# Optimization experiments

Hardware: AMD Instinct MI355X
Metric: run time of the kernel (lower is better)

The kernel has to match this reference:

```python
import jax, jax.numpy as jnp
import numpy as np

D = 1024      # d_model
ED = 2048     # d_inner
K = 4         # d_conv
N = 16        # d_state
R = 64        # dt_rank
E = 8         # num_experts
TOPK = 2      # num_experts_per_tok
FF = 2048     # mlp_size
EPS = 1e-6
B, L = 1, 2048


def setup_inputs() -> dict:
    key = jax.random.key(0)
    ks = jax.random.split(key, 12)
    def nrm(k, shape, scale=0.02):
        return jax.random.normal(k, shape, jnp.float32) * scale
    return {
        "x": jax.random.normal(ks[0], (B, L, D), jnp.float32),
        "rms1_w": jnp.ones((D,), jnp.float32),
        "rms2_w": jnp.ones((D,), jnp.float32),
        "W_in": nrm(ks[1], (2 * ED, D)),
        "conv_w": nrm(ks[2], (ED, 1, K), 0.1),
        "conv_b": jnp.zeros((ED,), jnp.float32),
        "W_xproj": nrm(ks[3], (R + 2 * N, ED)),
        "W_dt": nrm(ks[4], (ED, R), 0.1),
        "b_dt": jnp.full((ED,), -4.6, jnp.float32),  # softplus(-4.6) ~ 0.01 init dt
        "A_log": jnp.log(jnp.tile(jnp.arange(1, N + 1, dtype=jnp.float32), (ED, 1))),  # S4D-real init
        "D_skip": jnp.ones((ED,), jnp.float32),
        "W_out": nrm(ks[5], (D, ED)),
        "W_router": nrm(ks[6], (E, D)),
        "gate_w": nrm(ks[7], (E, FF, D)),
        "up_w": nrm(ks[8], (E, FF, D)),
        "down_w": nrm(ks[9], (E, D, FF)),
    }


def rmsnorm(x, w):
    return x * jax.lax.rsqrt(jnp.mean(x * x, -1, keepdims=True) + EPS) * w


def mamba(x, W_in, conv_w, conv_b, W_xproj, W_dt, b_dt, A_log, D_skip, W_out):
    Bb, Ll, _ = x.shape
    xm, z = jnp.split(x @ W_in.T, 2, axis=-1)                 # [B,L,ED] each
    # depthwise causal conv over time
    xc = jax.lax.conv_general_dilated(xm.transpose(0, 2, 1), conv_w, (1,), [(K - 1, 0)],
                                      feature_group_count=ED)  # [B,ED,L]
    xc = jax.nn.silu((xc + conv_b[None, :, None]).transpose(0, 2, 1))  # [B,L,ED]
    dt, Bm, Cm = jnp.split(xc @ W_xproj.T, [R, R + N], axis=-1)        # [B,L,R],[B,L,N],[B,L,N]
    delta = jax.nn.softplus(dt @ W_dt.T + b_dt)                        # [B,L,ED]
    A = -jnp.exp(A_log)                                                # [ED,N]
    dA = jnp.exp(delta[..., None] * A)                                 # [B,L,ED,N]
    dBx = delta[..., None] * Bm[:, :, None, :] * xc[..., None]         # [B,L,ED,N]

    def step(h, t):
        dA_t, dBx_t, C_t = t
        h = dA_t * h + dBx_t
        return h, jnp.einsum("ben,bn->be", h, C_t)

    h0 = jnp.zeros((Bb, ED, N), x.dtype)
    _, ys = jax.lax.scan(step, h0, (dA.transpose(1, 0, 2, 3), dBx.transpose(1, 0, 2, 3), Cm.transpose(1, 0, 2)))
    y = ys.transpose(1, 0, 2) + D_skip * xc
    y = y * jax.nn.silu(z)
    return y @ W_out.T


def moe(x2d, W_router, gate_w, up_w, down_w):
    logits = x2d @ W_router.T                                  # [T,E]
    probs = jax.nn.softmax(logits.astype(jnp.float32), -1)
    topw, sel = jax.lax.top_k(probs, TOPK)                     # NOTE: no renormalization (faithful)
    topw = topw.astype(x2d.dtype)
    wmat = jnp.sum(jax.nn.one_hot(sel, E, dtype=x2d.dtype) * topw[..., None], axis=1)  # [T,E]
    g = jnp.einsum("td,efd->tef", x2d, gate_w)
    u = jnp.einsum("td,efd->tef", x2d, up_w)
    h = jax.nn.silu(g) * u
    ye = jnp.einsum("tef,edf->ted", h, down_w)
    out = jnp.einsum("ted,te->td", ye, wmat)
    return out, logits


def reference(x, rms1_w, rms2_w, W_in, conv_w, conv_b, W_xproj, W_dt, b_dt, A_log,
              D_skip, W_out, W_router, gate_w, up_w, down_w):
    Bb, Ll, Dd = x.shape
    res = x
    h = rmsnorm(x, rms1_w)
    h = mamba(h, W_in, conv_w, conv_b, W_xproj, W_dt, b_dt, A_log, D_skip, W_out)
    x = res + h
    res = x
    h = rmsnorm(x, rms2_w)
    mo, logits = moe(h.reshape(-1, Dd), W_router, gate_w, up_w, down_w)
    x = res + mo.reshape(Bb, Ll, Dd)
    return (x, logits)
```

## Files before the change

kernel.cpp:

```cpp
#include <hip/hip_runtime.h>
#include <math.h>

typedef unsigned short u16;
typedef unsigned int   u32;
typedef __attribute__((ext_vector_type(8))) short bf16x8;
typedef __attribute__((ext_vector_type(4))) float f32x4;

constexpr int Tn=2048, Dm=1024, EDc=2048, Ns=16, Rr=64, NEx=8, FFc=2048;
constexpr int SCH=32, SNCH=Tn/SCH;
constexpr int MAXTM=40;
constexpr int MAXTM2=24;
constexpr float LOG2E = 1.44269504f;

__device__ __forceinline__ float siluf(float x){ return __fdividef(x, 1.f + __expf(-x)); }
__device__ __forceinline__ u16 bfr(float f){
  u32 u = __float_as_uint(f);
  return (u16)((u + 0x7fffu + ((u>>16)&1u)) >> 16);
}
__device__ __forceinline__ float b2f(u16 h){ return __uint_as_float(((u32)h)<<16); }

__device__ __forceinline__ void gload16(const void* g, void* l){
  __builtin_amdgcn_global_load_lds((const __attribute__((address_space(1))) void*)g,
                                   (__attribute__((address_space(3))) void*)l, 16, 0, 0);
}

__global__ __launch_bounds__(256) void f2b_k(const float* __restrict__ in,
                                             u16* __restrict__ out, int n4){
  int i = blockIdx.x*256 + threadIdx.x;
  if (i >= n4) return;
  float4 v = ((const float4*)in)[i];
  u32 lo = (u32)bfr(v.x) | ((u32)bfr(v.y)<<16);
  u32 hi = (u32)bfr(v.z) | ((u32)bfr(v.w)<<16);
  ((uint2*)out)[i] = make_uint2(lo, hi);
}

__global__ __launch_bounds__(256) void f2b3_k(
    const float* __restrict__ g, const float* __restrict__ u,
    const float* __restrict__ d,
    u16* __restrict__ og, u16* __restrict__ ou, u16* __restrict__ od){
  const int BPW = (NEx*FFc*Dm/4)/256;
  int b = blockIdx.x;
  int which = b / BPW;
  int i = (b - which*BPW)*256 + threadIdx.x;
  const float* in = (which==0) ? g : (which==1) ? u : d;
  u16* out        = (which==0) ? og : (which==1) ? ou : od;
  float4 v = ((const float4*)in)[i];
  u32 lo = (u32)bfr(v.x) | ((u32)bfr(v.y)<<16);
  u32 hi = (u32)bfr(v.z) | ((u32)bfr(v.w)<<16);
  ((uint2*)out)[i] = make_uint2(lo, hi);
}

__global__ __launch_bounds__(256) void rmsnorm_k(const float* __restrict__ x,
                                                 const float* __restrict__ w,
                                                 u16* __restrict__ ob){
  int t = blockIdx.x;
  const float* xr = x + (size_t)t * Dm;
  float v[4]; float s = 0.f;
#pragma unroll
  for (int j = 0; j < 4; j++){ int d = threadIdx.x + j*256; v[j] = xr[d]; s += v[j]*v[j]; }
#pragma unroll
  for (int m = 1; m < 64; m <<= 1) s += __shfl_xor(s, m);
  __shared__ float red[4]; __shared__ float sb;
  int lane = threadIdx.x & 63, wv = threadIdx.x >> 6;
  if (lane == 0) red[wv] = s;
  __syncthreads();
  if (threadIdx.x == 0) sb = rsqrtf((red[0]+red[1]+red[2]+red[3]) * (1.f/Dm) + 1e-6f);
  __syncthreads();
  float sc = sb;
#pragma unroll
  for (int j = 0; j < 4; j++){
    int d = threadIdx.x + j*256;
    ob[(size_t)t*Dm + d] = bfr(v[j]*sc*w[d]);
  }
}

__global__ __launch_bounds__(256) void rms2red_k(
  const float* __restrict__ x, const float* __restrict__ P,
  const float* __restrict__ w,
  float* __restrict__ out, float* __restrict__ h2f, u16* __restrict__ h2b)
{
  int t = blockIdx.x, tid = threadIdx.x;
  const size_t S = (size_t)Tn*Dm;
  float v[4]; float s = 0.f;
#pragma unroll
  for (int j = 0; j < 4; j++){
    int d = tid + j*256;
    size_t idx = (size_t)t*Dm + d;
    float a = x[idx] + ((P[idx] + P[S+idx]) + (P[2*S+idx] + P[3*S+idx]));
    out[idx] = a; v[j] = a; s += a*a;
  }
#pragma unroll
  for (int m = 1; m < 64; m <<= 1) s += __shfl_xor(s, m);
  __shared__ float red[4]; __shared__ float sb;
  int lane = tid & 63, wv = tid >> 6;
  if (lane == 0) red[wv] = s;
  __syncthreads();
  if (tid == 0) sb = rsqrtf((red[0]+red[1]+red[2]+red[3]) * (1.f/Dm) + 1e-6f);
  __syncthreads();
  float sc = sb;
#pragma unroll
  for (int j = 0; j < 4; j++){
    int d = tid + j*256;
    float o = v[j]*sc*w[d];
    h2b[(size_t)t*Dm + d] = bfr(o);
    h2f[(size_t)t*Dm + d] = o;
  }
}

template<int EPI, int OB>
__global__ __launch_bounds__(512) void gemm_bb(
    const u16* __restrict__ A, int lda,
    const u16* __restrict__ B, int ldb,
    void* __restrict__ Cv, int ldc,
    int M, int N, int Ksl, const float* __restrict__ aux)
{
  __shared__ u16 As[2*4096], Bs[2*4096];
  int tid = threadIdx.x, lane = tid & 63, wid = tid >> 6;
  int wr = wid >> 2, wc = wid & 3;
  int n0 = blockIdx.x * 128, m0 = blockIdx.y * 128;
  int r = tid >> 2;
  int kk = ((tid & 3) ^ (r & 3)) * 8;
  size_t kbeg = (size_t)blockIdx.z * Ksl;
  const u16* Ag = A + (size_t)min(m0 + r, M-1)*lda + kbeg + kk;
  const u16* Bg = B + (size_t)min(n0 + r, N-1)*ldb + kbeg + kk;
  f32x4 acc[4][2] = {};
  int sw = ((lane>>4) ^ (lane&3)) * 8;
  int aoff[4], boff[2];
#pragma unroll
  for (int i = 0; i < 4; i++) aoff[i] = (wr*64 + i*16 + (lane&15))*32 + sw;
#pragma unroll
  for (int j = 0; j < 2; j++) boff[j] = (wc*32 + j*16 + (lane&15))*32 + sw;
  gload16(Ag, As + tid*8);
  gload16(Bg, Bs + tid*8);
  int NT = Ksl >> 5;
  for (int kt = 0; kt < NT; kt++){
    int cur = (kt & 1) * 4096;
    if (kt + 1 < NT){
      int nxt = 4096 - cur;
      gload16(Ag + (size_t)(kt+1)*32, As + nxt + tid*8);
      gload16(Bg + (size_t)(kt+1)*32, Bs + nxt + tid*8);
      asm volatile("s_waitcnt vmcnt(2)" ::: "memory");
    } else {
      asm volatile("s_waitcnt vmcnt(0)" ::: "memory");
    }
    __builtin_amdgcn_s_barrier();
    bf16x8 af[4], bv[2];
#pragma unroll
    for (int i = 0; i < 4; i++) af[i] = *(const bf16x8*)&As[cur + aoff[i]];
#pragma unroll
    for (int j = 0; j < 2; j++) bv[j] = *(const bf16x8*)&Bs[cur + boff[j]];
    asm volatile("s_waitcnt lgkmcnt(0)" ::: "memory");
    __builtin_amdgcn_sched_barrier(0);
    __builtin_amdgcn_s_barrier();
    __builtin_amdgcn_s_setprio(1);
#pragma unroll
    for (int i = 0; i < 4; i++)
#pragma unroll
      for (int j = 0; j < 2; j++)
        acc[i][j] = __builtin_amdgcn_mfma_f32_16x16x32_bf16(af[i], bv[j], acc[i][j], 0,0,0);
    __builtin_amdgcn_s_setprio(0);
  }
  float* Cf = (float*)Cv + (size_t)blockIdx.z * M * ldc;
  u16*   Cb = (u16*)Cv;
#pragma unroll
  for (int i = 0; i < 4; i++){
    int rbase = m0 + wr*64 + i*16 + ((lane>>4)<<2);
#pragma unroll
    for (int j = 0; j < 2; j++){
      int col = n0 + wc*32 + j*16 + (lane&15);
      if (col >= N) continue;
#pragma unroll
      for (int q = 0; q < 4; q++){
        int row = rbase + q;
        if (row >= M) continue;
        float v = acc[i][j][q];
        if (EPI == 1){ v += aux[col]; v = (v > 20.f) ? v : __logf(1.f + __expf(v)); }
        if (OB) Cb[(size_t)row*ldc + col] = bfr(v);
        else    Cf[(size_t)row*ldc + col] = v;
      }
    }
  }
}

__global__ __launch_bounds__(512) void gateup8(
    const u16* __restrict__ Aall,
    const u16* __restrict__ Wg, const u16* __restrict__ Wu,
    const int* __restrict__ cnt, const int* __restrict__ off,
    const int* __restrict__ bucket,
    const int* __restrict__ tmap, const int* __restrict__ ntot,
    u16* __restrict__ H)
{
  if ((int)blockIdx.y >= *ntot) return;
  int v = tmap[blockIdx.y];
  int e = v >> 16, m0 = (v & 0xFFFF) * 256;
  int Me = cnt[e];
  __shared__ u16 As[2*8192], Gs[2*2048], Us[2*2048];
  int tid = threadIdx.x, lane = tid & 63, wid = tid >> 6;
  int wr = wid >> 1, wc = wid & 1;
  int n0 = blockIdx.x * 64;
  int r = tid >> 2;
  int kk = ((tid & 3) ^ (r & 3)) * 8;
  int arow  = bucket[e*Tn + min(m0 + r,       Me-1)];
  int arow2 = bucket[e*Tn + min(m0 + 128 + r, Me-1)];
  const u16* Ag  = Aall + (size_t)arow *Dm + kk;
  const u16* Ag2 = Aall + (size_t)arow2*Dm + kk;
  int rg = r & 63;
  const u16* GUg = ((tid < 256) ? Wg : Wu) + ((size_t)e*FFc + n0 + rg)*Dm + kk;
  u16* GUsb = (tid < 256) ? (u16*)Gs : (u16*)Us;
  int g8 = (tid & 255) * 8;
  f32x4 ag[4][2] = {}, au[4][2] = {};
  int sw = ((lane>>4) ^ (lane&3)) * 8;
  int aoff[4], boff[2];
#pragma unroll
  for (int i = 0; i < 4; i++) aoff[i] = (wr*64 + i*16 + (lane&15))*32 + sw;
#pragma unroll
  for (int j = 0; j < 2; j++) boff[j] = (wc*32 + j*16 + (lane&15))*32 + sw;
  const int NT = Dm >> 5;
  gload16(Ag,  As + tid*8);
  gload16(Ag2, As + 4096 + tid*8);
  gload16(GUg, GUsb + g8);
  for (int kt = 0; kt < NT; kt++){
    int cab = (kt & 1) * 8192, cgu = (kt & 1) * 2048;
    if (kt + 1 < NT){
      int nab = 8192 - cab, ngu = 2048 - cgu;
      gload16(Ag  + (size_t)(kt+1)*32, As + nab + tid*8);
      gload16(Ag2 + (size_t)(kt+1)*32, As + nab + 4096 + tid*8);
      gload16(GUg + (size_t)(kt+1)*32, GUsb + ngu + g8);
      asm volatile("s_waitcnt vmcnt(3)" ::: "memory");
    } else {
      asm volatile("s_waitcnt vmcnt(0)" ::: "memory");
    }
    __builtin_amdgcn_s_barrier();
    bf16x8 af[4], gf[2], uf[2];
#pragma unroll
    for (int i = 0; i < 4; i++) af[i] = *(const bf16x8*)&As[cab + aoff[i]];
#pragma unroll
    for (int j = 0; j < 2; j++){ gf[j] = *(const bf16x8*)&Gs[cgu + boff[j]];
                                 uf[j] = *(const bf16x8*)&Us[cgu + boff[j]]; }
    asm volatile("s_waitcnt lgkmcnt(0)" ::: "memory");
    __builtin_amdgcn_sched_barrier(0);
    __builtin_amdgcn_s_barrier();
    __builtin_amdgcn_s_setprio(1);
#pragma unroll
    for (int i = 0; i < 4; i++)
#pragma unroll
      for (int j = 0; j < 2; j++){
        ag[i][j] = __builtin_amdgcn_mfma_f32_16x16x32_bf16(af[i], gf[j], ag[i][j], 0,0,0);
        au[i][j] = __builtin_amdgcn_mfma_f32_16x16x32_bf16(af[i], uf[j], au[i][j], 0,0,0);
      }
    __builtin_amdgcn_s_setprio(0);
  }
  int offe = off[e];
#pragma unroll
  for (int i = 0; i < 4; i++){
    int mb = m0 + wr*64 + i*16 + ((lane>>4)<<2);
#pragma unroll
    for (int j = 0; j < 2; j++){
      int col = n0 + wc*32 + j*16 + (lane&15);
#pragma unroll
      for (int q = 0; q < 4; q++){
        int m = mb + q;
        if (m >= Me) continue;
        float g = ag[i][j][q], u = au[i][j][q];
        H[(size_t)(offe + m)*FFc + col] = bfr(siluf(g)*u);
      }
    }
  }
}

__global__ __launch_bounds__(512) void down8(
    const u16* __restrict__ Hall, const u16* __restrict__ Wd,
    const int* __restrict__ cnt, const int* __restrict__ off,
    const int* __restrict__ tmap2, const int* __restrict__ ntot2,
    u16* __restrict__ Y)
{
  if ((int)blockIdx.y >= *ntot2) return;
  int v = tmap2[blockIdx.y];
  int e = v >> 16, m0 = (v & 0xFFFF) * 128;
  int Me = cnt[e];
  int offe = off[e];
  int kbeg = blockIdx.z * (FFc/2);
  const u16* A = Hall + (size_t)offe*FFc;
  const u16* B = Wd + (size_t)e*Dm*FFc;
  u16* C = Y + (size_t)blockIdx.z*(2*Tn)*Dm + (size_t)offe*Dm;
  __shared__ u16 As[2*4096], Bs[2*4096];
  int tid = threadIdx.x, lane = tid & 63, wid = tid >> 6;
  int wr = wid >> 2, wc = wid & 3;
  int n0 = blockIdx.x * 128;
  int r = tid >> 2;
  int kk = ((tid & 3) ^ (r & 3)) * 8;
  const u16* Ag = A + (size_t)min(m0 + r, Me-1)*FFc + kbeg + kk;
  const u16* Bg = B + (size_t)(n0 + r)*FFc + kbeg + kk;
  f32x4 acc[4][2] = {};
  int sw = ((lane>>4) ^ (lane&3)) * 8;
  int aoff[4], boff[2];
#pragma unroll
  for (int i = 0; i < 4; i++) aoff[i] = (wr*64 + i*16 + (lane&15))*32 + sw;
#pragma unroll
  for (int j = 0; j < 2; j++) boff[j] = (wc*32 + j*16 + (lane&15))*32 + sw;
  gload16(Ag, As + tid*8);
  gload16(Bg, Bs + tid*8);
  const int NT = (FFc/2) >> 5;
  for (int kt = 0; kt < NT; kt++){
    int cur = (kt & 1) * 4096;
    if (kt + 1 < NT){
      int nxt = 4096 - cur;
      gload16(Ag + (size_t)(kt+1)*32, As + nxt + tid*8);
      gload16(Bg + (size_t)(kt+1)*32, Bs + nxt + tid*8);
      asm volatile("s_waitcnt vmcnt(2)" ::: "memory");
    } else {
      asm volatile("s_waitcnt vmcnt(0)" ::: "memory");
    }
    __builtin_amdgcn_s_barrier();
    bf16x8 af[4], bv[2];
#pragma unroll
    for (int i = 0; i < 4; i++) af[i] = *(const bf16x8*)&As[cur + aoff[i]];
#pragma unroll
    for (int j = 0; j < 2; j++) bv[j] = *(const bf16x8*)&Bs[cur + boff[j]];
    asm volatile("s_waitcnt lgkmcnt(0)" ::: "memory");
    __builtin_amdgcn_sched_barrier(0);
    __builtin_amdgcn_s_barrier();
    __builtin_amdgcn_s_setprio(1);
#pragma unroll
    for (int i = 0; i < 4; i++)
#pragma unroll
      for (int j = 0; j < 2; j++)
        acc[i][j] = __builtin_amdgcn_mfma_f32_16x16x32_bf16(af[i], bv[j], acc[i][j], 0,0,0);
    __builtin_amdgcn_s_setprio(0);
  }
#pragma unroll
  for (int i = 0; i < 4; i++){
    int mb = m0 + wr*64 + i*16 + ((lane>>4)<<2);
#pragma unroll
    for (int j = 0; j < 2; j++){
      int col = n0 + wc*32 + j*16 + (lane&15);
#pragma unroll
      for (int q = 0; q < 4; q++){
        int m = mb + q;
        if (m >= Me) continue;
        C[(size_t)m*Dm + col] = bfr(acc[i][j][q]);
      }
    }
  }
}

__global__ __launch_bounds__(256) void conv_k(const u16* __restrict__ xzb,
    const float* __restrict__ cw, const float* __restrict__ cb,
    u16* __restrict__ xc)
{
  int idx = blockIdx.x*256 + threadIdx.x;
  int t = idx >> 11, e = idx & (EDc - 1);
  float v = cb[e];
#pragma unroll
  for (int k = 0; k < 4; k++){
    int tt = t - 3 + k;
    if (tt >= 0) v += b2f(xzb[(size_t)tt*(2*EDc) + e]) * cw[e*4 + k];
  }
  xc[(size_t)t*EDc + e] = bfr(siluf(v));
}

__global__ __launch_bounds__(256) void xp_red(const float* __restrict__ part,
                                              float* __restrict__ xp,
                                              u16* __restrict__ dtA){
  int i = blockIdx.x*256 + threadIdx.x;
  const int S = Tn*96;
  float v = part[i] + part[S + i] + part[2*S + i] + part[3*S + i];
  xp[i] = v;
  int t = i / 96, c = i - t*96;
  if (c < Rr) dtA[t*Rr + c] = bfr(v);
}

__global__ __launch_bounds__(256) void scan_p1(
  const u16* __restrict__ delta, const u16* __restrict__ xc,
  const float* __restrict__ xp,  const float* __restrict__ A_log,
  float* __restrict__ hend, float* __restrict__ dsum)
{
  __shared__ u16 sdel[SCH*256], sxc[SCH*256];
  __shared__ float sB[SCH*16];
  int tid = threadIdx.x;
  int e0 = blockIdx.x*256, c = blockIdx.y, t0 = c*SCH;
#pragma unroll
  for (int i = 0; i < 4; i++){
    int f = (i*256+tid)*8;
    int t = f >> 8, e = f & 255;
    gload16(&delta[(size_t)(t0+t)*EDc + e0 + e], sdel + f);
    gload16(&xc  [(size_t)(t0+t)*EDc + e0 + e], sxc + f);
  }
  sB[tid]       = xp[(size_t)(t0 + (tid>>4))*96 + Rr + (tid&15)];
  sB[tid+256]   = xp[(size_t)(t0 + ((tid+256)>>4))*96 + Rr + (tid&15)];
  float a2[16];
  {
    const float* ar = &A_log[(size_t)(e0+tid)*16];
#pragma unroll
    for (int n = 0; n < 16; n++) a2[n] = -__expf(ar[n]) * LOG2E;
  }
  __syncthreads();
  float h[16] = {};
  float ds = 0.f;
  for (int t = 0; t < SCH; t++){
    float del = b2f(sdel[t*256 + tid]);
    float xv  = b2f(sxc [t*256 + tid]);
    ds += del;
    float dbx = del * xv;
    float4 b0 = *(const float4*)&sB[t*16];
    float4 b1 = *(const float4*)&sB[t*16+4];
    float4 b2 = *(const float4*)&sB[t*16+8];
    float4 b3 = *(const float4*)&sB[t*16+12];
    float bb[16] = {b0.x,b0.y,b0.z,b0.w, b1.x,b1.y,b1.z,b1.w,
                    b2.x,b2.y,b2.z,b2.w, b3.x,b3.y,b3.z,b3.w};
#pragma unroll
    for (int n = 0; n < 16; n++){
      float dA = exp2f(del * a2[n]);
      h[n] = fmaf(dA, h[n], dbx * bb[n]);
    }
  }
  float* hp = &hend[((size_t)c*EDc + e0 + tid)*16];
#pragma unroll
  for (int n = 0; n < 16; n += 4)
    *(float4*)&hp[n] = make_float4(h[n], h[n+1], h[n+2], h[n+3]);
  dsum[c*EDc + e0 + tid] = ds;
}

__global__ __launch_bounds__(256) void scan_p2(
  const float* __restrict__ hend, const float* __restrict__ dsum,
  const float* __restrict__ A_log, float* __restrict__ hin)
{
  int g = blockIdx.x*256 + threadIdx.x;
  int e = g >> 4;
  float a2 = -__expf(A_log[g]) * LOG2E;
  float h = 0.f;
  for (int c = 0; c < SNCH; c++){
    hin[(size_t)c*EDc*Ns + g] = h;
    float P = exp2f(a2 * dsum[c*EDc + e]);
    h = fmaf(P, h, hend[(size_t)c*EDc*Ns + g]);
  }
}

__global__ __launch_bounds__(256) void scan_p3(
  const u16* __restrict__ delta, const u16* __restrict__ xc,
  const float* __restrict__ xp,  const u16* __restrict__ xzb,
  const float* __restrict__ A_log, const float* __restrict__ D_skip,
  const float* __restrict__ hin,   u16* __restrict__ y2)
{
  __shared__ u16 sdel[SCH*256], sxc[SCH*256], sz[SCH*256];
  __shared__ float sB[SCH*16], sC[SCH*16];
  int tid = threadIdx.x;
  int e0 = blockIdx.x*256, c = blockIdx.y, t0 = c*SCH;
#pragma unroll
  for (int i = 0; i < 4; i++){
    int f = (i*256+tid)*8;
    int t = f >> 8, e = f & 255;
    gload16(&delta[(size_t)(t0+t)*EDc + e0 + e], sdel + f);
    gload16(&xc  [(size_t)(t0+t)*EDc + e0 + e], sxc + f);
    gload16(&xzb [(size_t)(t0+t)*(2*EDc) + EDc + e0 + e], sz + f);
  }
  {
    int f0 = tid, f1 = tid + 256;
    sB[f0] = xp[(size_t)(t0 + (f0>>4))*96 + Rr + (f0&15)];
    sB[f1] = xp[(size_t)(t0 + (f1>>4))*96 + Rr + (f1&15)];
    sC[f0] = xp[(size_t)(t0 + (f0>>4))*96 + Rr + Ns + (f0&15)];
    sC[f1] = xp[(size_t)(t0 + (f1>>4))*96 + Rr + Ns + (f1&15)];
  }
  float a2[16];
  {
    const float* ar = &A_log[(size_t)(e0+tid)*16];
#pragma unroll
    for (int n = 0; n < 16; n++) a2[n] = -__expf(ar[n]) * LOG2E;
  }
  float dsk = D_skip[e0 + tid];
  float h[16];
  {
    const float* hp = &hin[((size_t)c*EDc + e0 + tid)*16];
#pragma unroll
    for (int n = 0; n < 16; n += 4){
      float4 hv = *(const float4*)&hp[n];
      h[n] = hv.x; h[n+1] = hv.y; h[n+2] = hv.z; h[n+3] = hv.w;
    }
  }
  __syncthreads();
  for (int t = 0; t < SCH; t++){
    float del = b2f(sdel[t*256 + tid]);
    float xv  = b2f(sxc [t*256 + tid]);
    float zv  = b2f(sz  [t*256 + tid]);
    float dbx = del * xv;
    float4 b0 = *(const float4*)&sB[t*16];
    float4 b1 = *(const float4*)&sB[t*16+4];
    float4 b2 = *(const float4*)&sB[t*16+8];
    float4 b3 = *(const float4*)&sB[t*16+12];
    float bb[16] = {b0.x,b0.y,b0.z,b0.w, b1.x,b1.y,b1.z,b1.w,
                    b2.x,b2.y,b2.z,b2.w, b3.x,b3.y,b3.z,b3.w};
    float4 c0 = *(const float4*)&sC[t*16];
    float4 c1 = *(const float4*)&sC[t*16+4];
    float4 c2 = *(const float4*)&sC[t*16+8];
    float4 c3 = *(const float4*)&sC[t*16+12];
    float cc[16] = {c0.x,c0.y,c0.z,c0.w, c1.x,c1.y,c1.z,c1.w,
                    c2.x,c2.y,c2.z,c2.w, c3.x,c3.y,c3.z,c3.w};
    float p0 = 0.f, p1 = 0.f, p2 = 0.f, p3 = 0.f;
#pragma unroll
    for (int n = 0; n < 16; n += 4){
      float dA0 = exp2f(del * a2[n]);
      float dA1 = exp2f(del * a2[n+1]);
      float dA2 = exp2f(del * a2[n+2]);
      float dA3 = exp2f(del * a2[n+3]);
      h[n]   = fmaf(dA0, h[n],   dbx * bb[n]);
      h[n+1] = fmaf(dA1, h[n+1], dbx * bb[n+1]);
      h[n+2] = fmaf(dA2, h[n+2], dbx * bb[n+2]);
      h[n+3] = fmaf(dA3, h[n+3], dbx * bb[n+3]);
      p0 = fmaf(h[n],   cc[n],   p0);
      p1 = fmaf(h[n+1], cc[n+1], p1);
      p2 = fmaf(h[n+2], cc[n+2], p2);
      p3 = fmaf(h[n+3], cc[n+3], p3);
    }
    float p = (p0 + p1) + (p2 + p3);
    y2[(size_t)(t0+t)*EDc + e0 + tid] = bfr((p + dsk*xv) * siluf(zv));
  }
}

__global__ __launch_bounds__(256) void route_k(
  const float* __restrict__ h2, const float* __restrict__ Wr,
  float* __restrict__ logits_out,
  int* __restrict__ cnt, int* __restrict__ bucket,
  int* __restrict__ tok_e, int* __restrict__ tok_idx, float* __restrict__ tok_w)
{
  int t = blockIdx.x, tid = threadIdx.x;
  float p[8] = {};
#pragma unroll
  for (int j = 0; j < 4; j++){
    int d = tid + j*256;
    float xv = h2[(size_t)t*Dm + d];
#pragma unroll
    for (int e = 0; e < 8; e++) p[e] += xv * Wr[e*Dm + d];
  }
#pragma unroll
  for (int e = 0; e < 8; e++)
#pragma unroll
    for (int m = 1; m < 64; m <<= 1) p[e] += __shfl_xor(p[e], m);
  __shared__ float part[4][8];
  __shared__ float lg[8];
  int lane = tid & 63, wv = tid >> 6;
  if (lane == 0)
#pragma unroll
    for (int e = 0; e < 8; e++) part[wv][e] = p[e];
  __syncthreads();
  if (tid < 8){
    float v = part[0][tid]+part[1][tid]+part[2][tid]+part[3][tid];
    lg[tid] = v;
    logits_out[(size_t)t*8 + tid] = v;
  }
  __syncthreads();
  if (tid == 0){
    float mx = lg[0];
#pragma unroll
    for (int e = 1; e < 8; e++) mx = fmaxf(mx, lg[e]);
    float ex[8], s = 0.f;
#pragma unroll
    for (int e = 0; e < 8; e++){ ex[e] = expf(lg[e] - mx); s += ex[e]; }
    float inv = 1.f / s;
    int i0 = 0; float b0 = ex[0]*inv;
#pragma unroll
    for (int e = 1; e < 8; e++){ float pe = ex[e]*inv; if (pe > b0){ b0 = pe; i0 = e; } }
    int i1 = -1; float b1 = -1e30f;
#pragma unroll
    for (int e = 0; e < 8; e++){ if (e == i0) continue; float pe = ex[e]*inv; if (pe > b1){ b1 = pe; i1 = e; } }
    int k0 = atomicAdd(&cnt[i0], 1); bucket[i0*Tn + k0] = t;
    int k1 = atomicAdd(&cnt[i1], 1); bucket[i1*Tn + k1] = t;
    tok_e[2*t] = i0;   tok_idx[2*t] = k0;   tok_w[2*t] = b0;
    tok_e[2*t+1] = i1; tok_idx[2*t+1] = k1; tok_w[2*t+1] = b1;
  }
}

__global__ void prefix_k(const int* __restrict__ cnt, int* __restrict__ off,
                         int* __restrict__ tmap, int* __restrict__ ntot,
                         int* __restrict__ tmap2, int* __restrict__ ntot2){
  if (threadIdx.x == 0 && blockIdx.x == 0){
    int s = 0;
    for (int e = 0; e < NEx; e++){ off[e] = s; s += cnt[e]; }
    int nt = 0;
    for (int e = 0; e < NEx; e++){
      int tiles = (cnt[e] + 255) >> 8;
      for (int tm = 0; tm < tiles; tm++) tmap[nt++] = (e << 16) | tm;
    }
    *ntot = nt;
    int n2 = 0;
    for (int e = 0; e < NEx; e++){
      int tiles = (cnt[e] + 127) >> 7;
      for (int tm = 0; tm < tiles; tm++) tmap2[n2++] = (e << 16) | tm;
    }
    *ntot2 = n2;
  }
}

__global__ __launch_bounds__(256) void combine_k(float* __restrict__ out,
    const u16* __restrict__ Y, const int* __restrict__ off,
    const int* __restrict__ tok_e, const int* __restrict__ tok_idx,
    const float* __restrict__ tok_w)
{
  int t = blockIdx.x, tid = threadIdx.x;
  const size_t S2 = (size_t)(2*Tn)*Dm;
  int e0 = tok_e[2*t],   e1 = tok_e[2*t+1];
  size_t r0 = (size_t)(off[e0] + tok_idx[2*t])*Dm;
  size_t r1 = (size_t)(off[e1] + tok_idx[2*t+1])*Dm;
  float w0 = tok_w[2*t], w1 = tok_w[2*t+1];
#pragma unroll
  for (int j = 0; j < 4; j++){
    int d = tid + j*256;
    float y0 = b2f(Y[r0 + d]) + b2f(Y[S2 + r0 + d]);
    float y1 = b2f(Y[r1 + d]) + b2f(Y[S2 + r1 + d]);
    out[(size_t)t*Dm + d] += w0*y0 + w1*y1;
  }
}

extern "C" void kernel_launch(void* const* d_in, const int* in_sizes, int n_in,
                              void* d_out, int out_size, void* d_ws, size_t ws_size,
                              hipStream_t stream) {
  const float* x      = (const float*)d_in[0];
  const float* rms1_w = (const float*)d_in[1];
  const float* rms2_w = (const float*)d_in[2];
  const float* W_in   = (const float*)d_in[3];
  const float* conv_w = (const float*)d_in[4];
  const float* conv_b = (const float*)d_in[5];
  const float* W_xprj = (const float*)d_in[6];
  const float* W_dt   = (const float*)d_in[7];
  const float* b_dt   = (const float*)d_in[8];
  const float* A_log  = (const float*)d_in[9];
  const float* D_skip = (const float*)d_in[10];
  const float* W_out  = (const float*)d_in[11];
  const float* W_rt   = (const float*)d_in[12];
  const float* gate_w = (const float*)d_in[13];
  const float* up_w   = (const float*)d_in[14];
  const float* down_w = (const float*)d_in[15];

  float* out        = (float*)d_out;
  float* logits_out = out + (size_t)Tn*Dm;

  uint8_t* base = (uint8_t*)d_ws;
  size_t o = 0;
  auto alloc = [&](size_t bytes) -> void* {
    void* p = base + o;
    o = (o + bytes + 255) & ~(size_t)255;
    return p;
  };
  float* h2f   = (float*)alloc((size_t)Tn*Dm*4);
  u16*   h2b   = (u16*)  alloc((size_t)Tn*Dm*2);
  u16*   hmoe  = (u16*)  alloc((size_t)2*Tn*FFc*2);
  u16*   yslot = (u16*)  alloc((size_t)2*(2*Tn)*Dm*2);
  int*   cnt     = (int*)alloc(64);
  int*   off     = (int*)alloc(64);
  int*   ntot    = (int*)alloc(64);
  int*   ntot2   = (int*)alloc(64);
  int*   tmap    = (int*)alloc(MAXTM2*4 + 192);
  int*   tmap2   = (int*)alloc(MAXTM*4 + 192);
  int*   bucket  = (int*)alloc((size_t)NEx*Tn*4);
  int*   tok_e   = (int*)alloc((size_t)2*Tn*4);
  int*   tok_idx = (int*)alloc((size_t)2*Tn*4);
  float* tok_w   = (float*)alloc((size_t)2*Tn*4);
  size_t oz = o;
  u16*   xzb   = (u16*)  alloc((size_t)Tn*2*EDc*2);
  u16*   delta = (u16*)  alloc((size_t)Tn*EDc*2);
  u16*   xc    = (u16*)  alloc((size_t)Tn*EDc*2);
  u16*   y2    = (u16*)  alloc((size_t)Tn*EDc*2);
  u16*   h1b   = (u16*)  alloc((size_t)Tn*Dm*2);
  u16*   dtA   = (u16*)  alloc((size_t)Tn*Rr*2);
  float* xp    = (float*)alloc((size_t)Tn*96*4);
  float* xp_part=(float*)alloc((size_t)4*Tn*96*4);
  float* hend  = (float*)alloc((size_t)SNCH*EDc*Ns*4);
  float* hin   = (float*)alloc((size_t)SNCH*EDc*Ns*4);
  float* dsum  = (float*)alloc((size_t)SNCH*EDc*4);
  float* wpart = (float*)xzb;
  u16* wgate = (u16*)(base + oz);
  u16* wup   = wgate + (size_t)NEx*FFc*Dm;
  u16* wdown = wup   + (size_t)NEx*FFc*Dm;
  u16* wbin  = (u16*)yslot;
  u16* wbout = wbin + (size_t)2*EDc*Dm;
  u16* wxp   = (u16*)hmoe;
  u16* wdt   = wxp + (size_t)96*EDc;

  f2b_k<<<(2*EDc*Dm/4)/256, 256, 0, stream>>>(W_in,   wbin,  2*EDc*Dm/4);
  f2b_k<<<(Dm*EDc/4)/256,   256, 0, stream>>>(W_out,  wbout, Dm*EDc/4);
  f2b_k<<<(96*EDc/4)/256,   256, 0, stream>>>(W_xprj, wxp,   96*EDc/4);
  f2b_k<<<(EDc*Rr/4)/256,   256, 0, stream>>>(W_dt,   wdt,   EDc*Rr/4);
  rmsnorm_k<<<Tn, 256, 0, stream>>>(x, rms1_w, h1b);
  gemm_bb<0,1><<<dim3(32,16,1), 512, 0, stream>>>(h1b, Dm, wbin, Dm, xzb, 2*EDc, Tn, 2*EDc, Dm, nullptr);
  conv_k<<<(Tn*EDc)/256, 256, 0, stream>>>(xzb, conv_w, conv_b, xc);
  gemm_bb<0,0><<<dim3(1,16,4), 512, 0, stream>>>(xc, EDc, wxp, EDc, xp_part, 96, Tn, 96, EDc/4, nullptr);
  xp_red<<<(Tn*96)/256, 256, 0, stream>>>(xp_part, xp, dtA);
  gemm_bb<1,1><<<dim3(16,16,1), 512, 0, stream>>>(dtA, Rr, wdt, Rr, delta, EDc, Tn, EDc, Rr, b_dt);
  scan_p1<<<dim3(EDc/256, SNCH), 256, 0, stream>>>(delta, xc, xp, A_log, hend, dsum);
  scan_p2<<<EDc*Ns/256, 256, 0, stream>>>(hend, dsum, A_log, hin);
  scan_p3<<<dim3(EDc/256, SNCH), 256, 0, stream>>>(delta, xc, xp, xzb, A_log, D_skip, hin, y2);
  gemm_bb<0,0><<<dim3(8,16,4), 512, 0, stream>>>(y2, EDc, wbout, EDc, wpart, Dm, Tn, Dm, EDc/4, nullptr);
  rms2red_k<<<Tn, 256, 0, stream>>>(x, wpart, rms2_w, out, h2f, h2b);
  f2b3_k<<<3*((NEx*FFc*Dm/4)/256), 256, 0, stream>>>(gate_w, up_w, down_w, wgate, wup, wdown);
  hipMemsetAsync(cnt, 0, 32, stream);
  route_k<<<Tn, 256, 0, stream>>>(h2f, W_rt, logits_out, cnt, bucket, tok_e, tok_idx, tok_w);
  prefix_k<<<1, 64, 0, stream>>>(cnt, off, tmap, ntot, tmap2, ntot2);
  gateup8<<<dim3(32, MAXTM2), 512, 0, stream>>>(h2b, wgate, wup, cnt, off, bucket, tmap, ntot, hmoe);
  down8<<<dim3(8, MAXTM, 2), 512, 0, stream>>>(hmoe, wdown, cnt, off, tmap2, ntot2, yslot);
  combine_k<<<Tn, 256, 0, stream>>>(out, yslot, off, tok_e, tok_idx, tok_w);
}
```

Measured before the change: 397.2 us.

## Load MoE A-operand fragments directly from global into registers, bypassing LDS

```diff
diff --git a/kernel.cpp b/kernel.cpp
--- a/kernel.cpp
+++ b/kernel.cpp
@@ -194,46 +194,51 @@
   int v = tmap[blockIdx.y];
   int e = v >> 16, m0 = (v & 0xFFFF) * 256;
   int Me = cnt[e];
-  __shared__ u16 As[2*8192], Gs[2*2048], Us[2*2048];
+  __shared__ u16 Gs[2*2048], Us[2*2048];
   int tid = threadIdx.x, lane = tid & 63, wid = tid >> 6;
   int wr = wid >> 1, wc = wid & 1;
   int n0 = blockIdx.x * 64;
   int r = tid >> 2;
   int kk = ((tid & 3) ^ (r & 3)) * 8;
-  int arow  = bucket[e*Tn + min(m0 + r,       Me-1)];
-  int arow2 = bucket[e*Tn + min(m0 + 128 + r, Me-1)];
-  const u16* Ag  = Aall + (size_t)arow *Dm + kk;
-  const u16* Ag2 = Aall + (size_t)arow2*Dm + kk;
   int rg = r & 63;
   const u16* GUg = ((tid < 256) ? Wg : Wu) + ((size_t)e*FFc + n0 + rg)*Dm + kk;
   u16* GUsb = (tid < 256) ? (u16*)Gs : (u16*)Us;
   int g8 = (tid & 255) * 8;
+  const u16 *Af0, *Af1, *Af2, *Af3;
+  {
+    int kf = (lane >> 4) * 8;
+    int c  = lane & 15;
+    int r0 = bucket[e*Tn + min(m0 + wr*64 +  0 + c, Me-1)];
+    int r1 = bucket[e*Tn + min(m0 + wr*64 + 16 + c, Me-1)];
+    int r2 = bucket[e*Tn + min(m0 + wr*64 + 32 + c, Me-1)];
+    int r3 = bucket[e*Tn + min(m0 + wr*64 + 48 + c, Me-1)];
+    Af0 = Aall + (size_t)r0*Dm + kf;
+    Af1 = Aall + (size_t)r1*Dm + kf;
+    Af2 = Aall + (size_t)r2*Dm + kf;
+    Af3 = Aall + (size_t)r3*Dm + kf;
+  }
   f32x4 ag[4][2] = {}, au[4][2] = {};
   int sw = ((lane>>4) ^ (lane&3)) * 8;
-  int aoff[4], boff[2];
-#pragma unroll
-  for (int i = 0; i < 4; i++) aoff[i] = (wr*64 + i*16 + (lane&15))*32 + sw;
+  int boff[2];
 #pragma unroll
   for (int j = 0; j < 2; j++) boff[j] = (wc*32 + j*16 + (lane&15))*32 + sw;
   const int NT = Dm >> 5;
-  gload16(Ag,  As + tid*8);
-  gload16(Ag2, As + 4096 + tid*8);
   gload16(GUg, GUsb + g8);
   for (int kt = 0; kt < NT; kt++){
-    int cab = (kt & 1) * 8192, cgu = (kt & 1) * 2048;
+    int cgu = (kt & 1) * 2048;
+    bf16x8 af0 = *(const bf16x8*)(Af0 + (size_t)kt*32);
+    bf16x8 af1 = *(const bf16x8*)(Af1 + (size_t)kt*32);
+    bf16x8 af2 = *(const bf16x8*)(Af2 + (size_t)kt*32);
+    bf16x8 af3 = *(const bf16x8*)(Af3 + (size_t)kt*32);
+    __builtin_amdgcn_sched_barrier(0);
     if (kt + 1 < NT){
-      int nab = 8192 - cab, ngu = 2048 - cgu;
-      gload16(Ag  + (size_t)(kt+1)*32, As + nab + tid*8);
-      gload16(Ag2 + (size_t)(kt+1)*32, As + nab + 4096 + tid*8);
-      gload16(GUg + (size_t)(kt+1)*32, GUsb + ngu + g8);
-      asm volatile("s_waitcnt vmcnt(3)" ::: "memory");
+      gload16(GUg + (size_t)(kt+1)*32, GUsb + (2048 - cgu) + g8);
+      asm volatile("s_waitcnt vmcnt(5)" ::: "memory");
     } else {
-      asm volatile("s_waitcnt vmcnt(0)" ::: "memory");
+      asm volatile("s_waitcnt vmcnt(4)" ::: "memory");
     }
     __builtin_amdgcn_s_barrier();
-    bf16x8 af[4], gf[2], uf[2];
-#pragma unroll
-    for (int i = 0; i < 4; i++) af[i] = *(const bf16x8*)&As[cab + aoff[i]];
+    bf16x8 gf[2], uf[2];
 #pragma unroll
     for (int j = 0; j < 2; j++){ gf[j] = *(const bf16x8*)&Gs[cgu + boff[j]];
                                  uf[j] = *(const bf16x8*)&Us[cgu + boff[j]]; }
@@ -242,12 +247,16 @@
     __builtin_amdgcn_s_barrier();
     __builtin_amdgcn_s_setprio(1);
 #pragma unroll
-    for (int i = 0; i < 4; i++)
-#pragma unroll
-      for (int j = 0; j < 2; j++){
-        ag[i][j] = __builtin_amdgcn_mfma_f32_16x16x32_bf16(af[i], gf[j], ag[i][j], 0,0,0);
-        au[i][j] = __builtin_amdgcn_mfma_f32_16x16x32_bf16(af[i], uf[j], au[i][j], 0,0,0);
-      }
+    for (int j = 0; j < 2; j++){
+      ag[0][j] = __builtin_amdgcn_mfma_f32_16x16x32_bf16(af0, gf[j], ag[0][j], 0,0,0);
+      au[0][j] = __builtin_amdgcn_mfma_f32_16x16x32_bf16(af0, uf[j], au[0][j], 0,0,0);
+      ag[1][j] = __builtin_amdgcn_mfma_f32_16x16x32_bf16(af1, gf[j], ag[1][j], 0,0,0);
+      au[1][j] = __builtin_amdgcn_mfma_f32_16x16x32_bf16(af1, uf[j], au[1][j], 0,0,0);
+      ag[2][j] = __builtin_amdgcn_mfma_f32_16x16x32_bf16(af2, gf[j], ag[2][j], 0,0,0);
+      au[2][j] = __builtin_amdgcn_mfma_f32_16x16x32_bf16(af2, uf[j], au[2][j], 0,0,0);
+      ag[3][j] = __builtin_amdgcn_mfma_f32_16x16x32_bf16(af3, gf[j], ag[3][j], 0,0,0);
+      au[3][j] = __builtin_amdgcn_mfma_f32_16x16x32_bf16(af3, uf[j], au[3][j], 0,0,0);
+    }
     __builtin_amdgcn_s_setprio(0);
   }
   int offe = off[e];
@@ -283,38 +292,44 @@
   const u16* A = Hall + (size_t)offe*FFc;
   const u16* B = Wd + (size_t)e*Dm*FFc;
   u16* C = Y + (size_t)blockIdx.z*(2*Tn)*Dm + (size_t)offe*Dm;
-  __shared__ u16 As[2*4096], Bs[2*4096];
+  __shared__ u16 Bs[2*4096];
   int tid = threadIdx.x, lane = tid & 63, wid = tid >> 6;
   int wr = wid >> 2, wc = wid & 3;
   int n0 = blockIdx.x * 128;
   int r = tid >> 2;
   int kk = ((tid & 3) ^ (r & 3)) * 8;
-  const u16* Ag = A + (size_t)min(m0 + r, Me-1)*FFc + kbeg + kk;
   const u16* Bg = B + (size_t)(n0 + r)*FFc + kbeg + kk;
+  const u16 *Af0, *Af1, *Af2, *Af3;
+  {
+    int kf = (lane >> 4) * 8;
+    int c  = lane & 15;
+    Af0 = A + (size_t)min(m0 + wr*64 +  0 + c, Me-1)*FFc + kbeg + kf;
+    Af1 = A + (size_t)min(m0 + wr*64 + 16 + c, Me-1)*FFc + kbeg + kf;
+    Af2 = A + (size_t)min(m0 + wr*64 + 32 + c, Me-1)*FFc + kbeg + kf;
+    Af3 = A + (size_t)min(m0 + wr*64 + 48 + c, Me-1)*FFc + kbeg + kf;
+  }
   f32x4 acc[4][2] = {};
   int sw = ((lane>>4) ^ (lane&3)) * 8;
-  int aoff[4], boff[2];
-#pragma unroll
-  for (int i = 0; i < 4; i++) aoff[i] = (wr*64 + i*16 + (lane&15))*32 + sw;
+  int boff[2];
 #pragma unroll
   for (int j = 0; j < 2; j++) boff[j] = (wc*32 + j*16 + (lane&15))*32 + sw;
-  gload16(Ag, As + tid*8);
+  const int NT = (FFc/2) >> 5;
   gload16(Bg, Bs + tid*8);
-  const int NT = (FFc/2) >> 5;
   for (int kt = 0; kt < NT; kt++){
     int cur = (kt & 1) * 4096;
+    bf16x8 af0 = *(const bf16x8*)(Af0 + (size_t)kt*32);
+    bf16x8 af1 = *(const bf16x8*)(Af1 + (size_t)kt*32);
+    bf16x8 af2 = *(const bf16x8*)(Af2 + (size_t)kt*32);
+    bf16x8 af3 = *(const bf16x8*)(Af3 + (size_t)kt*32);
+    __builtin_amdgcn_sched_barrier(0);
     if (kt + 1 < NT){
-      int nxt = 4096 - cur;
-      gload16(Ag + (size_t)(kt+1)*32, As + nxt + tid*8);
-      gload16(Bg + (size_t)(kt+1)*32, Bs + nxt + tid*8);
-      asm volatile("s_waitcnt vmcnt(2)" ::: "memory");
+      gload16(Bg + (size_t)(kt+1)*32, Bs + (4096 - cur) + tid*8);
+      asm volatile("s_waitcnt vmcnt(5)" ::: "memory");
     } else {
-      asm volatile("s_waitcnt vmcnt(0)" ::: "memory");
+      asm volatile("s_waitcnt vmcnt(4)" ::: "memory");
     }
     __builtin_amdgcn_s_barrier();
-    bf16x8 af[4], bv[2];
-#pragma unroll
-    for (int i = 0; i < 4; i++) af[i] = *(const bf16x8*)&As[cur + aoff[i]];
+    bf16x8 bv[2];
 #pragma unroll
     for (int j = 0; j < 2; j++) bv[j] = *(const bf16x8*)&Bs[cur + boff[j]];
     asm volatile("s_waitcnt lgkmcnt(0)" ::: "memory");
@@ -322,10 +337,12 @@
     __builtin_amdgcn_s_barrier();
     __builtin_amdgcn_s_setprio(1);
 #pragma unroll
-    for (int i = 0; i < 4; i++)
-#pragma unroll
-      for (int j = 0; j < 2; j++)
-        acc[i][j] = __builtin_amdgcn_mfma_f32_16x16x32_bf16(af[i], bv[j], acc[i][j], 0,0,0);
+    for (int j = 0; j < 2; j++){
+      acc[0][j] = __builtin_amdgcn_mfma_f32_16x16x32_bf16(af0, bv[j], acc[0][j], 0,0,0);
+      acc[1][j] = __builtin_amdgcn_mfma_f32_16x16x32_bf16(af1, bv[j], acc[1][j], 0,0,0);
+      acc[2][j] = __builtin_amdgcn_mfma_f32_16x16x32_bf16(af2, bv[j], acc[2][j], 0,0,0);
+      acc[3][j] = __builtin_amdgcn_mfma_f32_16x16x32_bf16(af3, bv[j], acc[3][j], 0,0,0);
+    }
     __builtin_amdgcn_s_setprio(0);
   }
 #pragma unroll
```

Result: slower. 484.7 us (+22.0%).
